# Optimization experiments

Measured on AMD Instinct MI355X. Metric: run time of the kernel, lower is better.

## Reference

```python
import jax, jax.numpy as jnp
import numpy as np

B, C, H, W = 2, 128, 64, 256
G, P, EXP = 8, 4, 2
D = C // G


def _conv1x1(x, w, b):
    # x: (b,c,h,w), w: (o,c), b: (o,)
    return jnp.einsum('bchw,oc->bohw', x, w) + b[None, :, None, None]


def _lin_sample(value, x):
    # value: (b,g,d,h,w); x: (b,g,p,h,w) pixel coords along W -> (b,g,d,p,h,w)
    Bv, Gv, Dv, Hv, Wv = value.shape
    Pv = x.shape[2]
    xc = jnp.clip(x, 0.0, Wv - 1.0)
    x0 = jnp.floor(xc)
    i0 = x0.astype(jnp.int32)
    i1 = jnp.minimum(i0 + 1, Wv - 1)
    t = (xc - x0)[:, :, None]  # (b,g,1,p,h,w)
    shape = (Bv, Gv, Dv, Pv, Hv, Wv)
    v = jnp.broadcast_to(value[:, :, :, None], shape)
    v0 = jnp.take_along_axis(v, jnp.broadcast_to(i0[:, :, None], shape), axis=-1)
    v1 = jnp.take_along_axis(v, jnp.broadcast_to(i1[:, :, None], shape), axis=-1)
    return v0 * (1.0 - t) + v1 * t


def _layernorm_c(x, g, b):
    mu = jnp.mean(x, axis=1, keepdims=True)
    var = jnp.mean((x - mu) ** 2, axis=1, keepdims=True)
    return (x - mu) * jax.lax.rsqrt(var + 1e-5) * g[None, :, None, None] + b[None, :, None, None]


def _forward(ml, mr, fl, fr, nl, nr, gml, gmr, cap, gap,
             wv, bv, wn, bn, woc, boc, wog, bog, wa, ba, wo, bo,
             lw, lb, w1, b1, w2, b2):
    mask = jnp.concatenate([gml, gmr], axis=0)   # (2B,1,H,W)
    q = jnp.concatenate([ml, mr], axis=0)        # (2B,C,H,W)
    ctx = jnp.concatenate([fr, fl], axis=0)      # cross: right feats for left queries
    geo = jnp.concatenate([nr, nl], axis=0)      # (2B,3,H,W)
    B2 = q.shape[0]
    # deformable 1D cross-attention (normal-guided)
    value = _conv1x1(ctx, wv, bv).reshape(B2, G, D, H, W)
    nfeat = _conv1x1(geo, wn, bn).reshape(B2, G, D, H, W)
    off_c = _conv1x1(q, woc, boc).reshape(B2, G, P, H, W)
    off_g = _conv1x1(q, wog, bog).reshape(B2, G, P, H, W)
    attn = jax.nn.softmax(_conv1x1(q, wa, ba).reshape(B2, G, 2 * P, H, W), axis=2)
    ctx_kp = jnp.clip(cap * (W - 1.0) + off_c, 0.0, W - 1.0)
    geo_kp = jnp.clip(gap * (W - 1.0) + off_g, 0.0, W - 1.0)
    s_ctx = _lin_sample(value, ctx_kp)           # (2B,G,D,P,H,W)
    s_geo = _lin_sample(nfeat, geo_kp)
    sampled = jnp.concatenate([s_ctx, s_geo], axis=3)  # (2B,G,D,2P,H,W)
    agg = jnp.einsum('bgdphw,bgphw->bgdhw', sampled, attn).reshape(B2, C, H, W)
    upd = _conv1x1(agg, wo, bo) * mask
    # residual + LayerNorm over channels + 1x1-conv FFN
    x = q + upd
    x = _layernorm_c(x, lw, lb)
    h1 = _conv1x1(x, w1, b1)
    x = x + _conv1x1(h1 * jax.nn.sigmoid(h1), w2, b2)
    return x, ctx_kp, geo_kp


def setup_inputs() -> dict:
    key = jax.random.key(0)
    ks = jax.random.split(key, 20)
    f32 = jnp.float32
    def n(k, shape, s=1.0):
        return jax.random.normal(k, shape, dtype=f32) * s
    return {
        'match_left': n(ks[0], (B, C, H, W)),
        'match_right': n(ks[1], (B, C, H, W)),
        'feat_left': n(ks[2], (B, C, H, W)),
        'feat_right': n(ks[3], (B, C, H, W)),
        'normal_left': n(ks[4], (B, 3, H, W)),
        'normal_right': n(ks[5], (B, 3, H, W)),
        'gate_mask_left': jax.random.uniform(ks[6], (B, 1, H, W), dtype=f32),
        'gate_mask_right': jax.random.uniform(ks[7], (B, 1, H, W), dtype=f32),
        'context_anchor_points': jax.random.uniform(ks[8], (2 * B, G, P, H, W), dtype=f32),
        'geometric_anchor_points': jax.random.uniform(ks[9], (2 * B, G, P, H, W), dtype=f32),
        'w_value': n(ks[10], (C, C), 0.02), 'b_value': jnp.zeros((C,), f32),
        'w_normal': n(ks[11], (C, 3), 0.02), 'b_normal': jnp.zeros((C,), f32),
        'w_off_ctx': n(ks[12], (G * P, C), 0.02), 'b_off_ctx': jnp.zeros((G * P,), f32),
        'w_off_geo': n(ks[13], (G * P, C), 0.02), 'b_off_geo': jnp.zeros((G * P,), f32),
        'w_attn': n(ks[14], (G * 2 * P, C), 0.02), 'b_attn': jnp.zeros((G * 2 * P,), f32),
        'w_out': n(ks[15], (C, C), 0.02), 'b_out': jnp.zeros((C,), f32),
        'ln_w': jnp.ones((C,), f32), 'ln_b': jnp.zeros((C,), f32),
        'w_ff1': n(ks[16], (EXP * C, C), 0.02), 'b_ff1': jnp.zeros((EXP * C,), f32),
        'w_ff2': n(ks[17], (C, EXP * C), 0.02), 'b_ff2': jnp.zeros((C,), f32),
    }


def reference(match_left, match_right, feat_left, feat_right, normal_left, normal_right,
              gate_mask_left, gate_mask_right, context_anchor_points, geometric_anchor_points,
              w_value, b_value, w_normal, b_normal, w_off_ctx, b_off_ctx, w_off_geo, b_off_geo,
              w_attn, b_attn, w_out, b_out, ln_w, ln_b, w_ff1, b_ff1, w_ff2, b_ff2):
    x, ckp, gkp = _forward(match_left, match_right, feat_left, feat_right, normal_left, normal_right,
                           gate_mask_left, gate_mask_right, context_anchor_points, geometric_anchor_points,
                           w_value, b_value, w_normal, b_normal, w_off_ctx, b_off_ctx, w_off_geo, b_off_geo,
                           w_attn, b_attn, w_out, b_out, ln_w, ln_b, w_ff1, b_ff1, w_ff2, b_ff2)
    ml, mr = jnp.split(x, 2, axis=0)
    return (ml, mr, ckp, gkp)
```

## Files before the change

kernel.cpp:

```cpp
#include <hip/hip_runtime.h>
#include <cstdint>
#include <math.h>

#define B2v 4
#define Cc  128
#define Hh  64
#define Ww  256
#define Gg  8
#define Pp  4
#define HW  (Hh*Ww)
#define CHW (Cc*HW)
#define PIT 136

typedef float f32x4 __attribute__((ext_vector_type(4)));
typedef float f32x2 __attribute__((ext_vector_type(2)));
typedef short s16x8 __attribute__((ext_vector_type(8)));
typedef short s16x4 __attribute__((ext_vector_type(4)));

__device__ __forceinline__ short f2bf(float x) {
    union { float f; unsigned u; } a; a.f = x;
    unsigned r = a.u + 0x7fffu + ((a.u >> 16) & 1u);
    return (short)(r >> 16);
}
__device__ __forceinline__ float bf2f(short s) {
    union { unsigned u; float f; } a; a.u = ((unsigned)(unsigned short)s) << 16;
    return a.f;
}
__device__ __forceinline__ unsigned cvtpk(float lo, float hi) {
    unsigned r;
    asm("v_cvt_pk_bf16_f32 %0, %1, %2" : "=v"(r) : "v"(lo), "v"(hi));
    return r;
}
__device__ __forceinline__ f32x2 unpk(unsigned w) {
    union { unsigned u; float f; } lo, hi;
    lo.u = w << 16; hi.u = w & 0xffff0000u;
    return (f32x2){lo.f, hi.f};
}
__device__ __forceinline__ float frcp(float x) { return __builtin_amdgcn_rcpf(x); }
__device__ __forceinline__ float fexp(float x) { return __expf(x); }

__global__ __launch_bounds__(256) void prep_kernel(
    const float* __restrict__ wv, const float* __restrict__ woc,
    const float* __restrict__ wog, const float* __restrict__ wa,
    const float* __restrict__ wo, const float* __restrict__ w1,
    const float* __restrict__ w2,
    const float* __restrict__ boc, const float* __restrict__ bog,
    const float* __restrict__ ba,
    short* __restrict__ wbf, float* __restrict__ bq)
{
    int i = blockIdx.x * 256 + threadIdx.x;
    if (i < 16384) wbf[i] = f2bf(wv[i]);
    else if (i < 32768) {
        int j = i - 16384; int r = j >> 7, c = j & 127;
        float v = (r < 32) ? woc[r * 128 + c] : (r < 64) ? wog[(r - 32) * 128 + c]
                                              : wa[(r - 64) * 128 + c];
        wbf[i] = f2bf(v);
    }
    else if (i < 49152)  wbf[i] = f2bf(wo[i - 32768]);
    else if (i < 81920)  wbf[i] = f2bf(w1[i - 49152]);
    else if (i < 114688) wbf[i] = f2bf(w2[i - 81920]);
    else if (i < 114816) {
        int r = i - 114688;
        bq[r] = (r < 32) ? boc[r] : (r < 64) ? bog[r - 32] : ba[r - 64];
    }
}

__global__ __launch_bounds__(512, 2) void mega_kernel(
    const float* __restrict__ mlq, const float* __restrict__ mrq,
    const float* __restrict__ fl,  const float* __restrict__ fr,
    const float* __restrict__ nl,  const float* __restrict__ nr,
    const float* __restrict__ gml, const float* __restrict__ gmr,
    const float* __restrict__ cap, const float* __restrict__ gap,
    const short* __restrict__ wbf, const float* __restrict__ bq,
    const float* __restrict__ bv,
    const float* __restrict__ wn,  const float* __restrict__ bn,
    const float* __restrict__ bo,
    const float* __restrict__ lnw, const float* __restrict__ lnb,
    const float* __restrict__ b1,  const float* __restrict__ b2,
    float* __restrict__ out_ml, float* __restrict__ out_mr,
    float* __restrict__ ckp_out, float* __restrict__ gkp_out)
{
    __shared__ short buf1[256 * PIT];
    __shared__ short buf2[256 * PIT];
    __shared__ f32x4 sgeo4[256];
    __shared__ f32x2 swnp[256];
    __shared__ float sln[256];
    __shared__ float redS[512], redQ[512];
    __shared__ float smu[256], srs[256];

    const short* wv_bf = wbf;
    const short* wq_bf = wbf + 16384;
    const short* wo_bf = wbf + 32768;
    const short* w1_bf = wbf + 49152;
    const short* w2_bf = wbf + 81920;

    const int t    = threadIdx.x;
    const int lane = t & 63;
    const int ww   = t >> 6;
    const int lm   = lane & 15;
    const int lq   = lane >> 4;
    const int h = blockIdx.x, b = blockIdx.y;
    const int hWw = h * Ww;
    const int px   = t & 255;
    const int half = t >> 8;

    const float* ctx = (b < 2) ? fr + (size_t)b * CHW : fl + (size_t)(b - 2) * CHW;
    const float* q   = (b < 2) ? mlq + (size_t)b * CHW : mrq + (size_t)(b - 2) * CHW;
    const float* geo = (b < 2) ? nr + (size_t)b * 3 * HW : nl + (size_t)(b - 2) * 3 * HW;
    const float* msk = (b < 2) ? gml + (size_t)b * HW : gmr + (size_t)(b - 2) * HW;
    float* outp = (b < 2) ? out_ml + (size_t)b * CHW : out_mr + (size_t)(b - 2) * CHW;

    float capr[16], gapr[16];
    const size_t kbase = ((size_t)b * Gg + half * 4) * Pp * (size_t)HW + hWw + px;
    {
#pragma unroll
        for (int i = 0; i < 16; i++) {
            capr[i] = cap[kbase + (size_t)i * HW];
            gapr[i] = gap[kbase + (size_t)i * HW];
        }
    }

    if (t < 256) {
        sgeo4[t] = (f32x4){geo[hWw + t], geo[HW + hWw + t], geo[2 * HW + hWw + t], 0.f};
        const int pr = t >> 2, m = t & 3;
        const int ch0 = pr * 2, ch1 = ch0 + 1;
        float a0 = (m < 3) ? wn[ch0 * 3 + m] : bn[ch0];
        float a1 = (m < 3) ? wn[ch1 * 3 + m] : bn[ch1];
        swnp[t] = (f32x2){a0, a1};
    }
    else {
        int i = t - 256;
        sln[i] = (i < 128) ? lnw[i] : lnb[i - 128];
    }

    {
        const int c0 = ww * 16;
        const int p0 = lane * 4;
        const size_t gbase = (size_t)c0 * HW + hWw + p0;
        {
            f32x4 L[16];
#pragma unroll
            for (int c = 0; c < 16; c++) L[c] = *(const f32x4*)(ctx + gbase + (size_t)c * HW);
#pragma unroll
            for (int j = 0; j < 4; j++) {
                uint4 w0, w1;
                w0.x = cvtpk(L[0][j],  L[1][j]);  w0.y = cvtpk(L[2][j],  L[3][j]);
                w0.z = cvtpk(L[4][j],  L[5][j]);  w0.w = cvtpk(L[6][j],  L[7][j]);
                w1.x = cvtpk(L[8][j],  L[9][j]);  w1.y = cvtpk(L[10][j], L[11][j]);
                w1.z = cvtpk(L[12][j], L[13][j]); w1.w = cvtpk(L[14][j], L[15][j]);
                *(uint4*)(&buf1[(p0 + j) * PIT + c0])     = w0;
                *(uint4*)(&buf1[(p0 + j) * PIT + c0 + 8]) = w1;
            }
        }
        {
            f32x4 L[16];
#pragma unroll
            for (int c = 0; c < 16; c++) L[c] = *(const f32x4*)(q + gbase + (size_t)c * HW);
#pragma unroll
            for (int j = 0; j < 4; j++) {
                uint4 w0, w1;
                w0.x = cvtpk(L[0][j],  L[1][j]);  w0.y = cvtpk(L[2][j],  L[3][j]);
                w0.z = cvtpk(L[4][j],  L[5][j]);  w0.w = cvtpk(L[6][j],  L[7][j]);
                w1.x = cvtpk(L[8][j],  L[9][j]);  w1.y = cvtpk(L[10][j], L[11][j]);
                w1.z = cvtpk(L[12][j], L[13][j]); w1.w = cvtpk(L[14][j], L[15][j]);
                *(uint4*)(&buf2[(p0 + j) * PIT + c0])     = w0;
                *(uint4*)(&buf2[(p0 + j) * PIT + c0 + 8]) = w1;
            }
        }
    }
    __syncthreads();

    f32x4 accv[16];
#pragma unroll
    for (int nt = 0; nt < 16; nt++) accv[nt] = (f32x4){0.f, 0.f, 0.f, 0.f};
#pragma unroll
    for (int kk = 0; kk < 4; kk++) {
        s16x8 a = *(const s16x8*)(wv_bf + (size_t)(ww * 16 + lm) * 128 + kk * 32 + lq * 8);
#pragma unroll
        for (int nt = 0; nt < 16; nt++) {
            s16x8 bfv = *(const s16x8*)(&buf1[(nt * 16 + lm) * PIT + kk * 32 + lq * 8]);
            accv[nt] = __builtin_amdgcn_mfma_f32_16x16x32_bf16(a, bfv, accv[nt], 0, 0, 0);
        }
    }
    __syncthreads();

    {
        const int ob = ww * 16 + lq * 4;
        float bias[4];
#pragma unroll
        for (int r = 0; r < 4; r++) bias[r] = bv[ob + r];
#pragma unroll
        for (int nt = 0; nt < 16; nt++) {
            const int wg = nt * 16 + lm;
            uint2 pk;
            pk.x = cvtpk(accv[nt][0] + bias[0], accv[nt][1] + bias[1]);
            pk.y = cvtpk(accv[nt][2] + bias[2], accv[nt][3] + bias[3]);
            *(uint2*)(&buf1[wg * PIT + ob]) = pk;
        }
    }
    f32x4 accp[16];
#pragma unroll
    for (int nt = 0; nt < 16; nt++) accp[nt] = (f32x4){0.f, 0.f, 0.f, 0.f};
#pragma unroll
    for (int kk = 0; kk < 4; kk++) {
        s16x8 a = *(const s16x8*)(wq_bf + (size_t)(ww * 16 + lm) * 128 + kk * 32 + lq * 8);
#pragma unroll
        for (int nt = 0; nt < 16; nt++) {
            s16x8 bfv = *(const s16x8*)(&buf2[(nt * 16 + lm) * PIT + kk * 32 + lq * 8]);
            accp[nt] = __builtin_amdgcn_mfma_f32_16x16x32_bf16(a, bfv, accp[nt], 0, 0, 0);
        }
    }
    __syncthreads();

    {
        const int ob = ww * 16 + lq * 4;
        float bias[4];
#pragma unroll
        for (int r = 0; r < 4; r++) bias[r] = bq[ob + r];
#pragma unroll
        for (int nt = 0; nt < 16; nt++) {
            const int wg = nt * 16 + lm;
            uint2 pk;
            pk.x = cvtpk(accp[nt][0] + bias[0], accp[nt][1] + bias[1]);
            pk.y = cvtpk(accp[nt][2] + bias[2], accp[nt][3] + bias[3]);
            *(uint2*)(&buf2[wg * PIT + ob]) = pk;
        }
    }
    __syncthreads();

    float attnr[4][8], kpr[4][8];
#pragma unroll
    for (int gi = 0; gi < 4; gi++) {
        const int g = half * 4 + gi;
        s16x8 lg = *(const s16x8*)(&buf2[px * PIT + 64 + g * 8]);
        float L[8], m = -1e30f;
#pragma unroll
        for (int j = 0; j < 8; j++) { L[j] = bf2f(lg[j]); m = fmaxf(m, L[j]); }
        float s = 0.f;
#pragma unroll
        for (int j = 0; j < 8; j++) { L[j] = fexp(L[j] - m); s += L[j]; }
        float inv = frcp(s);
#pragma unroll
        for (int j = 0; j < 8; j++) attnr[gi][j] = L[j] * inv;
#pragma unroll
        for (int p = 0; p < 4; p++) {
            size_t kidx = kbase + (size_t)(gi * 4 + p) * HW;
            float oc = bf2f(buf2[px * PIT + g * 4 + p]);
            float og = bf2f(buf2[px * PIT + 32 + g * 4 + p]);
            float ck = fminf(fmaxf(capr[gi * 4 + p] * 255.0f + oc, 0.f), 255.f);
            float gk = fminf(fmaxf(gapr[gi * 4 + p] * 255.0f + og, 0.f), 255.f);
            ckp_out[kidx] = ck;
            gkp_out[kidx] = gk;
            kpr[gi][p] = ck;
            kpr[gi][4 + p] = gk;
        }
    }
    __syncthreads();

#pragma unroll
    for (int gi = 0; gi < 4; gi++) {
        const int g = half * 4 + gi;
        f32x2 A[8];
#pragma unroll
        for (int k = 0; k < 8; k++) A[k] = (f32x2){0.f, 0.f};
#pragma unroll
        for (int j = 0; j < 4; j++) {
            float x = kpr[gi][j];
            float fx = floorf(x);
            int i0 = (int)fx;
            int i1 = min(i0 + 1, Ww - 1);
            float tt = x - fx;
            float c0 = attnr[gi][j] * (1.f - tt);
            float c1 = attnr[gi][j] * tt;
            f32x2 c0v = {c0, c0}, c1v = {c1, c1};
            uint4 v0a = *(const uint4*)(&buf1[i0 * PIT + g * 16]);
            uint4 v0b = *(const uint4*)(&buf1[i0 * PIT + g * 16 + 8]);
            uint4 v1a = *(const uint4*)(&buf1[i1 * PIT + g * 16]);
            uint4 v1b = *(const uint4*)(&buf1[i1 * PIT + g * 16 + 8]);
            const unsigned w0[8] = {v0a.x, v0a.y, v0a.z, v0a.w, v0b.x, v0b.y, v0b.z, v0b.w};
            const unsigned w1[8] = {v1a.x, v1a.y, v1a.z, v1a.w, v1b.x, v1b.y, v1b.z, v1b.w};
#pragma unroll
            for (int k = 0; k < 8; k++)
                A[k] += unpk(w0[k]) * c0v + unpk(w1[k]) * c1v;
        }
        {
            float gs0 = 0.f, gs1 = 0.f, gs2 = 0.f, as = 0.f;
#pragma unroll
            for (int j = 4; j < 8; j++) {
                float x = kpr[gi][j];
                float fx = floorf(x);
                int i0 = (int)fx;
                int i1 = min(i0 + 1, Ww - 1);
                float tt = x - fx;
                float c0 = attnr[gi][j] * (1.f - tt);
                float c1 = attnr[gi][j] * tt;
                f32x4 ga = sgeo4[i0], gb = sgeo4[i1];
                gs0 += c0 * ga[0] + c1 * gb[0];
                gs1 += c0 * ga[1] + c1 * gb[1];
                gs2 += c0 * ga[2] + c1 * gb[2];
                as  += attnr[gi][j];
            }
            f32x2 g0v = {gs0, gs0}, g1v = {gs1, gs1}, g2v = {gs2, gs2}, asv = {as, as};
#pragma unroll
            for (int k = 0; k < 8; k++) {
                const f32x2* wp = &swnp[(g * 8 + k) * 4];
                A[k] += wp[0] * g0v + wp[1] * g1v + wp[2] * g2v + wp[3] * asv;
            }
        }
        uint4 o0, o1;
        o0.x = cvtpk(A[0][0], A[0][1]); o0.y = cvtpk(A[1][0], A[1][1]);
        o0.z = cvtpk(A[2][0], A[2][1]); o0.w = cvtpk(A[3][0], A[3][1]);
        o1.x = cvtpk(A[4][0], A[4][1]); o1.y = cvtpk(A[5][0], A[5][1]);
        o1.z = cvtpk(A[6][0], A[6][1]); o1.w = cvtpk(A[7][0], A[7][1]);
        *(uint4*)(&buf2[px * PIT + g * 16])     = o0;
        *(uint4*)(&buf2[px * PIT + g * 16 + 8]) = o1;
    }
    __syncthreads();

    {
        f32x4 acc1[16];
#pragma unroll
        for (int nt = 0; nt < 16; nt++) acc1[nt] = (f32x4){0.f, 0.f, 0.f, 0.f};
#pragma unroll
        for (int kk = 0; kk < 4; kk++) {
            s16x8 a = *(const s16x8*)(wo_bf + (size_t)(ww * 16 + lm) * 128 + kk * 32 + lq * 8);
#pragma unroll
            for (int nt = 0; nt < 16; nt++) {
                s16x8 bfv = *(const s16x8*)(&buf2[(nt * 16 + lm) * PIT + kk * 32 + lq * 8]);
                acc1[nt] = __builtin_amdgcn_mfma_f32_16x16x32_bf16(a, bfv, acc1[nt], 0, 0, 0);
            }
        }
        const int ob = ww * 16 + lq * 4;
        float bias[4];
#pragma unroll
        for (int r = 0; r < 4; r++) bias[r] = bo[ob + r];
#pragma unroll
        for (int nt = 0; nt < 16; nt++) {
            const int wg = nt * 16 + lm;
            float mval = msk[hWw + wg];
            float xv[4];
#pragma unroll
            for (int r = 0; r < 4; r++) {
                float upd = acc1[nt][r] + bias[r];
                float qv = q[(size_t)(ob + r) * HW + hWw + wg];
                xv[r] = qv + upd * mval;
            }
            uint2 pk;
            pk.x = cvtpk(xv[0], xv[1]);
            pk.y = cvtpk(xv[2], xv[3]);
            *(uint2*)(&buf1[wg * PIT + ob]) = pk;
        }
    }
    __syncthreads();

    {
        float ls = 0.f, lsq = 0.f;
#pragma unroll
        for (int c8 = 0; c8 < 8; c8++) {
            uint4 u = *(const uint4*)(&buf1[px * PIT + half * 64 + c8 * 8]);
            const unsigned wv4[4] = {u.x, u.y, u.z, u.w};
#pragma unroll
            for (int j2 = 0; j2 < 4; j2++) {
                f32x2 e = unpk(wv4[j2]);
                ls  += e[0] + e[1];
                lsq += e[0] * e[0] + e[1] * e[1];
            }
        }
        redS[t] = ls; redQ[t] = lsq;
        __syncthreads();
        if (t < 256) {
            float s  = redS[t] + redS[t + 256];
            float qq = redQ[t] + redQ[t + 256];
            float mu = s * (1.f / 128.f);
            float var = qq * (1.f / 128.f) - mu * mu;
            smu[t] = mu;
            srs[t] = __builtin_amdgcn_rsqf(var + 1e-5f);
        }
        __syncthreads();
        const float mu = smu[px], rs = srs[px];
#pragma unroll
        for (int c8 = 0; c8 < 8; c8++) {
            const int cb = half * 64 + c8 * 8;
            uint4 u = *(const uint4*)(&buf1[px * PIT + cb]);
            const unsigned wv4[4] = {u.x, u.y, u.z, u.w};
            uint4 o;
            unsigned res[4];
#pragma unroll
            for (int j2 = 0; j2 < 4; j2++) {
                f32x2 e = unpk(wv4[j2]);
                const int c = cb + j2 * 2;
                float a0 = rs * sln[c],     bb0 = sln[128 + c]     - mu * a0;
                float a1 = rs * sln[c + 1], bb1 = sln[128 + c + 1] - mu * a1;
                res[j2] = cvtpk(e[0] * a0 + bb0, e[1] * a1 + bb1);
            }
            o.x = res[0]; o.y = res[1]; o.z = res[2]; o.w = res[3];
            *(uint4*)(&buf1[px * PIT + cb]) = o;
        }
    }
    __syncthreads();

    f32x4 acc3[16];
#pragma unroll
    for (int nt = 0; nt < 16; nt++) acc3[nt] = (f32x4){0.f, 0.f, 0.f, 0.f};

    for (int jc = 0; jc < 2; jc++) {
        f32x4 acc2[16];
#pragma unroll
        for (int nt = 0; nt < 16; nt++) acc2[nt] = (f32x4){0.f, 0.f, 0.f, 0.f};
#pragma unroll
        for (int kk = 0; kk < 4; kk++) {
            s16x8 a = *(const s16x8*)(w1_bf + (size_t)(jc * 128 + ww * 16 + lm) * 128 + kk * 32 + lq * 8);
#pragma unroll
            for (int nt = 0; nt < 16; nt++) {
                s16x8 bfv = *(const s16x8*)(&buf1[(nt * 16 + lm) * PIT + kk * 32 + lq * 8]);
                acc2[nt] = __builtin_amdgcn_mfma_f32_16x16x32_bf16(a, bfv, acc2[nt], 0, 0, 0);
            }
        }
        {
            const int jb = ww * 16 + lq * 4;
            float bias[4];
#pragma unroll
            for (int r = 0; r < 4; r++) bias[r] = b1[jc * 128 + jb + r];
#pragma unroll
            for (int nt = 0; nt < 16; nt++) {
                const int wg = nt * 16 + lm;
                float o[4];
#pragma unroll
                for (int r = 0; r < 4; r++) {
                    float hv = acc2[nt][r] + bias[r];
                    o[r] = hv * frcp(1.f + fexp(-hv));
                }
                uint2 pk;
                pk.x = cvtpk(o[0], o[1]);
                pk.y = cvtpk(o[2], o[3]);
                *(uint2*)(&buf2[wg * PIT + jb]) = pk;
            }
        }
        __syncthreads();
#pragma unroll
        for (int kk = 0; kk < 4; kk++) {
            s16x8 a = *(const s16x8*)(w2_bf + (size_t)(ww * 16 + lm) * 256 + jc * 128 + kk * 32 + lq * 8);
#pragma unroll
            for (int nt = 0; nt < 16; nt++) {
                s16x8 bfv = *(const s16x8*)(&buf2[(nt * 16 + lm) * PIT + kk * 32 + lq * 8]);
                acc3[nt] = __builtin_amdgcn_mfma_f32_16x16x32_bf16(a, bfv, acc3[nt], 0, 0, 0);
            }
        }
        __syncthreads();
    }

    {
        const int ob = ww * 16 + lq * 4;
        float b2v[4];
#pragma unroll
        for (int r = 0; r < 4; r++) b2v[r] = b2[ob + r];
#pragma unroll
        for (int nt = 0; nt < 16; nt++) {
            const int wg = nt * 16 + lm;
            s16x4 xn4 = *(const s16x4*)(&buf1[wg * PIT + ob]);
#pragma unroll
            for (int r = 0; r < 4; r++)
                outp[(size_t)(ob + r) * HW + hWw + wg] = bf2f(xn4[r]) + b2v[r] + acc3[nt][r];
        }
    }
}

extern "C" void kernel_launch(void* const* d_in, const int* in_sizes, int n_in,
                              void* d_out, int out_size, void* d_ws, size_t ws_size,
                              hipStream_t stream)
{
    const float* match_l = (const float*)d_in[0];
    const float* match_r = (const float*)d_in[1];
    const float* feat_l  = (const float*)d_in[2];
    const float* feat_r  = (const float*)d_in[3];
    const float* norm_l  = (const float*)d_in[4];
    const float* norm_r  = (const float*)d_in[5];
    const float* gml     = (const float*)d_in[6];
    const float* gmr     = (const float*)d_in[7];
    const float* cap     = (const float*)d_in[8];
    const float* gap     = (const float*)d_in[9];
    const float* wv  = (const float*)d_in[10]; const float* bv  = (const float*)d_in[11];
    const float* wn  = (const float*)d_in[12]; const float* bn  = (const float*)d_in[13];
    const float* woc = (const float*)d_in[14]; const float* boc = (const float*)d_in[15];
    const float* wog = (const float*)d_in[16]; const float* bog = (const float*)d_in[17];
    const float* wa  = (const float*)d_in[18]; const float* ba  = (const float*)d_in[19];
    const float* wo  = (const float*)d_in[20]; const float* bo  = (const float*)d_in[21];
    const float* lnw = (const float*)d_in[22]; const float* lnb = (const float*)d_in[23];
    const float* w1  = (const float*)d_in[24]; const float* b1  = (const float*)d_in[25];
    const float* w2  = (const float*)d_in[26]; const float* b2  = (const float*)d_in[27];

    float* out = (float*)d_out;
    float* out_ml  = out;
    float* out_mr  = out + (size_t)2 * CHW;
    float* ckp_out = out + (size_t)4 * CHW;
    float* gkp_out = ckp_out + (size_t)B2v * Gg * Pp * HW;

    float* ws = (float*)d_ws;
    float* bq  = ws;
    short* wbf = (short*)(bq + 128);

    prep_kernel<<<dim3(449), dim3(256), 0, stream>>>(
        wv, woc, wog, wa, wo, w1, w2, boc, bog, ba, wbf, bq);
    mega_kernel<<<dim3(Hh, B2v), dim3(512), 0, stream>>>(
        match_l, match_r, feat_l, feat_r, norm_l, norm_r, gml, gmr, cap, gap,
        wbf, bq, bv, wn, bn, bo, lnw, lnb, b1, b2,
        out_ml, out_mr, ckp_out, gkp_out);
}
```

Measured before the change: 206.8 us.

## Double block to 1024 threads, splitting pixel tiles and groups across 16 waves

Grows the fused kernel's block from 8 to 16 waves. Each wave now owns one 16-row output slice and half of the pixel tiles in every MFMA GEMM. The sampling, softmax and layernorm phases are split four ways across pixels instead of two, and the reduction arrays grow to match. The goal is more waves per CU to hide memory and LDS latency, and fewer accumulator registers per thread. In exchange, the tighter launch bounds may cap VGPRs and cause spills, and each weight fragment is loaded twice per block.

```diff
diff --git a/kernel.cpp b/kernel.cpp
--- a/kernel.cpp
+++ b/kernel.cpp
@@ -65,7 +65,7 @@
     }
 }
 
-__global__ __launch_bounds__(512, 2) void mega_kernel(
+__global__ __launch_bounds__(1024, 4) void mega_kernel(
     const float* __restrict__ mlq, const float* __restrict__ mrq,
     const float* __restrict__ fl,  const float* __restrict__ fr,
     const float* __restrict__ nl,  const float* __restrict__ nr,
@@ -85,7 +85,7 @@
     __shared__ f32x4 sgeo4[256];
     __shared__ f32x2 swnp[256];
     __shared__ float sln[256];
-    __shared__ float redS[512], redQ[512];
+    __shared__ float redS[1024], redQ[1024];
     __shared__ float smu[256], srs[256];
 
     const short* wv_bf = wbf;
@@ -96,13 +96,15 @@
 
     const int t    = threadIdx.x;
     const int lane = t & 63;
-    const int ww   = t >> 6;
+    const int wvid = t >> 6;
+    const int rw   = wvid & 7;
+    const int pw   = wvid >> 3;
     const int lm   = lane & 15;
     const int lq   = lane >> 4;
     const int h = blockIdx.x, b = blockIdx.y;
     const int hWw = h * Ww;
     const int px   = t & 255;
-    const int half = t >> 8;
+    const int qt   = t >> 8;
 
     const float* ctx = (b < 2) ? fr + (size_t)b * CHW : fl + (size_t)(b - 2) * CHW;
     const float* q   = (b < 2) ? mlq + (size_t)b * CHW : mrq + (size_t)(b - 2) * CHW;
@@ -110,11 +112,11 @@
     const float* msk = (b < 2) ? gml + (size_t)b * HW : gmr + (size_t)(b - 2) * HW;
     float* outp = (b < 2) ? out_ml + (size_t)b * CHW : out_mr + (size_t)(b - 2) * CHW;
 
-    float capr[16], gapr[16];
-    const size_t kbase = ((size_t)b * Gg + half * 4) * Pp * (size_t)HW + hWw + px;
-    {
-#pragma unroll
-        for (int i = 0; i < 16; i++) {
+    float capr[8], gapr[8];
+    const size_t kbase = ((size_t)b * Gg + qt * 2) * Pp * (size_t)HW + hWw + px;
+    {
+#pragma unroll
+        for (int i = 0; i < 8; i++) {
             capr[i] = cap[kbase + (size_t)i * HW];
             gapr[i] = gap[kbase + (size_t)i * HW];
         }
@@ -128,98 +130,92 @@
         float a1 = (m < 3) ? wn[ch1 * 3 + m] : bn[ch1];
         swnp[t] = (f32x2){a0, a1};
     }
-    else {
+    else if (t < 512) {
         int i = t - 256;
         sln[i] = (i < 128) ? lnw[i] : lnb[i - 128];
     }
 
     {
-        const int c0 = ww * 16;
+        const int c0 = wvid * 8;
         const int p0 = lane * 4;
         const size_t gbase = (size_t)c0 * HW + hWw + p0;
         {
-            f32x4 L[16];
-#pragma unroll
-            for (int c = 0; c < 16; c++) L[c] = *(const f32x4*)(ctx + gbase + (size_t)c * HW);
+            f32x4 L[8];
+#pragma unroll
+            for (int c = 0; c < 8; c++) L[c] = *(const f32x4*)(ctx + gbase + (size_t)c * HW);
 #pragma unroll
             for (int j = 0; j < 4; j++) {
-                uint4 w0, w1;
-                w0.x = cvtpk(L[0][j],  L[1][j]);  w0.y = cvtpk(L[2][j],  L[3][j]);
-                w0.z = cvtpk(L[4][j],  L[5][j]);  w0.w = cvtpk(L[6][j],  L[7][j]);
-                w1.x = cvtpk(L[8][j],  L[9][j]);  w1.y = cvtpk(L[10][j], L[11][j]);
-                w1.z = cvtpk(L[12][j], L[13][j]); w1.w = cvtpk(L[14][j], L[15][j]);
-                *(uint4*)(&buf1[(p0 + j) * PIT + c0])     = w0;
-                *(uint4*)(&buf1[(p0 + j) * PIT + c0 + 8]) = w1;
+                uint4 w0;
+                w0.x = cvtpk(L[0][j], L[1][j]);  w0.y = cvtpk(L[2][j], L[3][j]);
+                w0.z = cvtpk(L[4][j], L[5][j]);  w0.w = cvtpk(L[6][j], L[7][j]);
+                *(uint4*)(&buf1[(p0 + j) * PIT + c0]) = w0;
             }
         }
         {
-            f32x4 L[16];
-#pragma unroll
-            for (int c = 0; c < 16; c++) L[c] = *(const f32x4*)(q + gbase + (size_t)c * HW);
+            f32x4 L[8];
+#pragma unroll
+            for (int c = 0; c < 8; c++) L[c] = *(const f32x4*)(q + gbase + (size_t)c * HW);
 #pragma unroll
             for (int j = 0; j < 4; j++) {
-                uint4 w0, w1;
-                w0.x = cvtpk(L[0][j],  L[1][j]);  w0.y = cvtpk(L[2][j],  L[3][j]);
-                w0.z = cvtpk(L[4][j],  L[5][j]);  w0.w = cvtpk(L[6][j],  L[7][j]);
-                w1.x = cvtpk(L[8][j],  L[9][j]);  w1.y = cvtpk(L[10][j], L[11][j]);
-                w1.z = cvtpk(L[12][j], L[13][j]); w1.w = cvtpk(L[14][j], L[15][j]);
-                *(uint4*)(&buf2[(p0 + j) * PIT + c0])     = w0;
-                *(uint4*)(&buf2[(p0 + j) * PIT + c0 + 8]) = w1;
-            }
-        }
-    }
-    __syncthreads();
-
-    f32x4 accv[16];
-#pragma unroll
-    for (int nt = 0; nt < 16; nt++) accv[nt] = (f32x4){0.f, 0.f, 0.f, 0.f};
+                uint4 w0;
+                w0.x = cvtpk(L[0][j], L[1][j]);  w0.y = cvtpk(L[2][j], L[3][j]);
+                w0.z = cvtpk(L[4][j], L[5][j]);  w0.w = cvtpk(L[6][j], L[7][j]);
+                *(uint4*)(&buf2[(p0 + j) * PIT + c0]) = w0;
+            }
+        }
+    }
+    __syncthreads();
+
+    f32x4 accv[8];
+#pragma unroll
+    for (int nt = 0; nt < 8; nt++) accv[nt] = (f32x4){0.f, 0.f, 0.f, 0.f};
 #pragma unroll
     for (int kk = 0; kk < 4; kk++) {
-        s16x8 a = *(const s16x8*)(wv_bf + (size_t)(ww * 16 + lm) * 128 + kk * 32 + lq * 8);
-#pragma unroll
-        for (int nt = 0; nt < 16; nt++) {
-            s16x8 bfv = *(const s16x8*)(&buf1[(nt * 16 + lm) * PIT + kk * 32 + lq * 8]);
+        s16x8 a = *(const s16x8*)(wv_bf + (size_t)(rw * 16 + lm) * 128 + kk * 32 + lq * 8);
+#pragma unroll
+        for (int nt = 0; nt < 8; nt++) {
+            s16x8 bfv = *(const s16x8*)(&buf1[((pw * 8 + nt) * 16 + lm) * PIT + kk * 32 + lq * 8]);
             accv[nt] = __builtin_amdgcn_mfma_f32_16x16x32_bf16(a, bfv, accv[nt], 0, 0, 0);
         }
     }
     __syncthreads();
 
     {
-        const int ob = ww * 16 + lq * 4;
+        const int ob = rw * 16 + lq * 4;
         float bias[4];
 #pragma unroll
         for (int r = 0; r < 4; r++) bias[r] = bv[ob + r];
 #pragma unroll
-        for (int nt = 0; nt < 16; nt++) {
-            const int wg = nt * 16 + lm;
+        for (int nt = 0; nt < 8; nt++) {
+            const int wg = (pw * 8 + nt) * 16 + lm;
             uint2 pk;
             pk.x = cvtpk(accv[nt][0] + bias[0], accv[nt][1] + bias[1]);
             pk.y = cvtpk(accv[nt][2] + bias[2], accv[nt][3] + bias[3]);
             *(uint2*)(&buf1[wg * PIT + ob]) = pk;
         }
     }
-    f32x4 accp[16];
-#pragma unroll
-    for (int nt = 0; nt < 16; nt++) accp[nt] = (f32x4){0.f, 0.f, 0.f, 0.f};
+    f32x4 accp[8];
+#pragma unroll
+    for (int nt = 0; nt < 8; nt++) accp[nt] = (f32x4){0.f, 0.f, 0.f, 0.f};
 #pragma unroll
     for (int kk = 0; kk < 4; kk++) {
-        s16x8 a = *(const s16x8*)(wq_bf + (size_t)(ww * 16 + lm) * 128 + kk * 32 + lq * 8);
-#pragma unroll
-        for (int nt = 0; nt < 16; nt++) {
-            s16x8 bfv = *(const s16x8*)(&buf2[(nt * 16 + lm) * PIT + kk * 32 + lq * 8]);
+        s16x8 a = *(const s16x8*)(wq_bf + (size_t)(rw * 16 + lm) * 128 + kk * 32 + lq * 8);
+#pragma unroll
+        for (int nt = 0; nt < 8; nt++) {
+            s16x8 bfv = *(const s16x8*)(&buf2[((pw * 8 + nt) * 16 + lm) * PIT + kk * 32 + lq * 8]);
             accp[nt] = __builtin_amdgcn_mfma_f32_16x16x32_bf16(a, bfv, accp[nt], 0, 0, 0);
         }
     }
     __syncthreads();
 
     {
-        const int ob = ww * 16 + lq * 4;
+        const int ob = rw * 16 + lq * 4;
         float bias[4];
 #pragma unroll
         for (int r = 0; r < 4; r++) bias[r] = bq[ob + r];
 #pragma unroll
-        for (int nt = 0; nt < 16; nt++) {
-            const int wg = nt * 16 + lm;
+        for (int nt = 0; nt < 8; nt++) {
+            const int wg = (pw * 8 + nt) * 16 + lm;
             uint2 pk;
             pk.x = cvtpk(accp[nt][0] + bias[0], accp[nt][1] + bias[1]);
             pk.y = cvtpk(accp[nt][2] + bias[2], accp[nt][3] + bias[3]);
@@ -228,10 +224,10 @@
     }
     __syncthreads();
 
-    float attnr[4][8], kpr[4][8];
-#pragma unroll
-    for (int gi = 0; gi < 4; gi++) {
-        const int g = half * 4 + gi;
+    float attnr[2][8], kpr[2][8];
+#pragma unroll
+    for (int gi = 0; gi < 2; gi++) {
+        const int g = qt * 2 + gi;
         s16x8 lg = *(const s16x8*)(&buf2[px * PIT + 64 + g * 8]);
         float L[8], m = -1e30f;
 #pragma unroll
@@ -258,8 +254,8 @@
     __syncthreads();
 
 #pragma unroll
-    for (int gi = 0; gi < 4; gi++) {
-        const int g = half * 4 + gi;
+    for (int gi = 0; gi < 2; gi++) {
+        const int g = qt * 2 + gi;
         f32x2 A[8];
 #pragma unroll
         for (int k = 0; k < 8; k++) A[k] = (f32x2){0.f, 0.f};
@@ -318,25 +314,25 @@
     __syncthreads();
 
     {
-        f32x4 acc1[16];
-#pragma unroll
-        for (int nt = 0; nt < 16; nt++) acc1[nt] = (f32x4){0.f, 0.f, 0.f, 0.f};
+        f32x4 acc1[8];
+#pragma unroll
+        for (int nt = 0; nt < 8; nt++) acc1[nt] = (f32x4){0.f, 0.f, 0.f, 0.f};
 #pragma unroll
         for (int kk = 0; kk < 4; kk++) {
-            s16x8 a = *(const s16x8*)(wo_bf + (size_t)(ww * 16 + lm) * 128 + kk * 32 + lq * 8);
-#pragma unroll
-            for (int nt = 0; nt < 16; nt++) {
-                s16x8 bfv = *(const s16x8*)(&buf2[(nt * 16 + lm) * PIT + kk * 32 + lq * 8]);
+            s16x8 a = *(const s16x8*)(wo_bf + (size_t)(rw * 16 + lm) * 128 + kk * 32 + lq * 8);
+#pragma unroll
+            for (int nt = 0; nt < 8; nt++) {
+                s16x8 bfv = *(const s16x8*)(&buf2[((pw * 8 + nt) * 16 + lm) * PIT + kk * 32 + lq * 8]);
                 acc1[nt] = __builtin_amdgcn_mfma_f32_16x16x32_bf16(a, bfv, acc1[nt], 0, 0, 0);
             }
         }
-        const int ob = ww * 16 + lq * 4;
+        const int ob = rw * 16 + lq * 4;
         float bias[4];
 #pragma unroll
         for (int r = 0; r < 4; r++) bias[r] = bo[ob + r];
 #pragma unroll
-        for (int nt = 0; nt < 16; nt++) {
-            const int wg = nt * 16 + lm;
+        for (int nt = 0; nt < 8; nt++) {
+            const int wg = (pw * 8 + nt) * 16 + lm;
             float mval = msk[hWw + wg];
             float xv[4];
 #pragma unroll
@@ -356,8 +352,8 @@
     {
         float ls = 0.f, lsq = 0.f;
 #pragma unroll
-        for (int c8 = 0; c8 < 8; c8++) {
-            uint4 u = *(const uint4*)(&buf1[px * PIT + half * 64 + c8 * 8]);
+        for (int c8 = 0; c8 < 4; c8++) {
+            uint4 u = *(const uint4*)(&buf1[px * PIT + qt * 32 + c8 * 8]);
             const unsigned wv4[4] = {u.x, u.y, u.z, u.w};
 #pragma unroll
             for (int j2 = 0; j2 < 4; j2++) {
@@ -369,8 +365,8 @@
         redS[t] = ls; redQ[t] = lsq;
         __syncthreads();
         if (t < 256) {
-            float s  = redS[t] + redS[t + 256];
-            float qq = redQ[t] + redQ[t + 256];
+            float s  = redS[t] + redS[t + 256] + redS[t + 512] + redS[t + 768];
+            float qq = redQ[t] + redQ[t + 256] + redQ[t + 512] + redQ[t + 768];
             float mu = s * (1.f / 128.f);
             float var = qq * (1.f / 128.f) - mu * mu;
             smu[t] = mu;
@@ -379,8 +375,8 @@
         __syncthreads();
         const float mu = smu[px], rs = srs[px];
 #pragma unroll
-        for (int c8 = 0; c8 < 8; c8++) {
-            const int cb = half * 64 + c8 * 8;
+        for (int c8 = 0; c8 < 4; c8++) {
+            const int cb = qt * 32 + c8 * 8;
             uint4 u = *(const uint4*)(&buf1[px * PIT + cb]);
             const unsigned wv4[4] = {u.x, u.y, u.z, u.w};
             uint4 o;
@@ -399,31 +395,31 @@
     }
     __syncthreads();
 
-    f32x4 acc3[16];
-#pragma unroll
-    for (int nt = 0; nt < 16; nt++) acc3[nt] = (f32x4){0.f, 0.f, 0.f, 0.f};
+    f32x4 acc3[8];
+#pragma unroll
+    for (int nt = 0; nt < 8; nt++) acc3[nt] = (f32x4){0.f, 0.f, 0.f, 0.f};
 
     for (int jc = 0; jc < 2; jc++) {
-        f32x4 acc2[16];
-#pragma unroll
-        for (int nt = 0; nt < 16; nt++) acc2[nt] = (f32x4){0.f, 0.f, 0.f, 0.f};
+        f32x4 acc2[8];
+#pragma unroll
+        for (int nt = 0; nt < 8; nt++) acc2[nt] = (f32x4){0.f, 0.f, 0.f, 0.f};
 #pragma unroll
         for (int kk = 0; kk < 4; kk++) {
-            s16x8 a = *(const s16x8*)(w1_bf + (size_t)(jc * 128 + ww * 16 + lm) * 128 + kk * 32 + lq * 8);
-#pragma unroll
-            for (int nt = 0; nt < 16; nt++) {
-                s16x8 bfv = *(const s16x8*)(&buf1[(nt * 16 + lm) * PIT + kk * 32 + lq * 8]);
+            s16x8 a = *(const s16x8*)(w1_bf + (size_t)(jc * 128 + rw * 16 + lm) * 128 + kk * 32 + lq * 8);
+#pragma unroll
+            for (int nt = 0; nt < 8; nt++) {
+                s16x8 bfv = *(const s16x8*)(&buf1[((pw * 8 + nt) * 16 + lm) * PIT + kk * 32 + lq * 8]);
                 acc2[nt] = __builtin_amdgcn_mfma_f32_16x16x32_bf16(a, bfv, acc2[nt], 0, 0, 0);
             }
         }
         {
-            const int jb = ww * 16 + lq * 4;
+            const int jb = rw * 16 + lq * 4;
             float bias[4];
 #pragma unroll
             for (int r = 0; r < 4; r++) bias[r] = b1[jc * 128 + jb + r];
 #pragma unroll
-            for (int nt = 0; nt < 16; nt++) {
-                const int wg = nt * 16 + lm;
+            for (int nt = 0; nt < 8; nt++) {
+                const int wg = (pw * 8 + nt) * 16 + lm;
                 float o[4];
 #pragma unroll
                 for (int r = 0; r < 4; r++) {
@@ -439,10 +435,10 @@
         __syncthreads();
 #pragma unroll
         for (int kk = 0; kk < 4; kk++) {
-            s16x8 a = *(const s16x8*)(w2_bf + (size_t)(ww * 16 + lm) * 256 + jc * 128 + kk * 32 + lq * 8);
-#pragma unroll
-            for (int nt = 0; nt < 16; nt++) {
-                s16x8 bfv = *(const s16x8*)(&buf2[(nt * 16 + lm) * PIT + kk * 32 + lq * 8]);
+            s16x8 a = *(const s16x8*)(w2_bf + (size_t)(rw * 16 + lm) * 256 + jc * 128 + kk * 32 + lq * 8);
+#pragma unroll
+            for (int nt = 0; nt < 8; nt++) {
+                s16x8 bfv = *(const s16x8*)(&buf2[((pw * 8 + nt) * 16 + lm) * PIT + kk * 32 + lq * 8]);
                 acc3[nt] = __builtin_amdgcn_mfma_f32_16x16x32_bf16(a, bfv, acc3[nt], 0, 0, 0);
             }
         }
@@ -450,13 +446,13 @@
     }
 
     {
-        const int ob = ww * 16 + lq * 4;
+        const int ob = rw * 16 + lq * 4;
         float b2v[4];
 #pragma unroll
         for (int r = 0; r < 4; r++) b2v[r] = b2[ob + r];
 #pragma unroll
-        for (int nt = 0; nt < 16; nt++) {
-            const int wg = nt * 16 + lm;
+        for (int nt = 0; nt < 8; nt++) {
+            const int wg = (pw * 8 + nt) * 16 + lm;
             s16x4 xn4 = *(const s16x4*)(&buf1[wg * PIT + ob]);
 #pragma unroll
             for (int r = 0; r < 4; r++)
@@ -501,7 +497,7 @@
 
     prep_kernel<<<dim3(449), dim3(256), 0, stream>>>(
         wv, woc, wog, wa, wo, w1, w2, boc, bog, ba, wbf, bq);
-    mega_kernel<<<dim3(Hh, B2v), dim3(512), 0, stream>>>(
+    mega_kernel<<<dim3(Hh, B2v), dim3(1024), 0, stream>>>(
         match_l, match_r, feat_l, feat_r, norm_l, norm_r, gml, gmr, cap, gap,
         wbf, bq, bv, wn, bn, bo, lnw, lnb, b1, b2,
         out_ml, out_mr, ckp_out, gkp_out);
```

New measurement: 213.8 us. +3.4%, slower.
